# Kernel tuning notes

Measured on AMD Instinct MI355X. Metric: run time of the kernel, lower is better.

The kernel has to match this reference:

```python
import jax, jax.numpy as jnp
import numpy as np

COMMITMENT_COST = 0.25
DIST_SCALE = 400.0


def setup_inputs() -> dict:
    key = jax.random.key(0)
    ks = jax.random.split(key, 6)
    B, T, D, K = 64, 1024, 512, 512
    s = 1.0 / np.sqrt(D)
    return {
        "inputs": jax.random.normal(ks[0], (B, T, D), dtype=jnp.float32),
        "mean_W": jax.random.normal(ks[1], (D, D), dtype=jnp.float32) * s,
        "mean_b": jax.random.normal(ks[2], (D,), dtype=jnp.float32) * s,
        "logvar_W": jax.random.normal(ks[3], (D, K), dtype=jnp.float32) * s,
        "logvar_b": jax.random.normal(ks[4], (K,), dtype=jnp.float32) * s,
        "embedding": jax.random.normal(ks[5], (K, D), dtype=jnp.float32),
    }


def reference(inputs, mean_W, mean_b, logvar_W, logvar_b, embedding):
    sg = jax.lax.stop_gradient
    D = embedding.shape[1]
    flat = inputs.reshape(-1, D)                      # [N, D]
    x = flat @ mean_W + mean_b                        # mean_layer, [N, D]
    z_logvar = x @ logvar_W + logvar_b                # logvar_layer, [N, K]
    # squared euclidean distances to codebook, [N, K]
    distances = (
        jnp.sum(x * x, axis=1, keepdims=True)
        + jnp.sum(embedding * embedding, axis=1)
        - 2.0 * (x @ embedding.T)
    )
    smooth = jnp.exp(-2.0 * z_logvar)                 # 1/exp(logvar)^2
    d = distances / DIST_SCALE
    prob = jnp.exp(-d * (0.5 * smooth)) / jnp.sqrt(smooth)
    probs = prob / jnp.sum(prob, axis=1, keepdims=True)  # per-row normalize, [N, K]
    quantized = (probs @ embedding).reshape(inputs.shape)
    e_latent_loss = jnp.mean((sg(quantized) - inputs) ** 2)
    q_latent_loss = jnp.mean((quantized - sg(inputs)) ** 2)
    loss = q_latent_loss + COMMITMENT_COST * e_latent_loss
    quantized_st = inputs + sg(quantized - inputs)    # straight-through
    avg_probs = jnp.mean(probs, axis=0)
    perplexity = jnp.exp(-jnp.sum(avg_probs * jnp.log(avg_probs + 1e-10)))
    return loss, quantized_st, perplexity, probs
```

## Files before the change

### kernel.cpp

```cpp
#include <hip/hip_runtime.h>
#include <stdint.h>

#define BM 128
#define BN 128
#define BK 32
#define DIMD 512
#define NROWS 65536
#define QOFF 1
#define PERPOFF 33554433
#define PROBSOFF 33554434
#define NELEM 33554432

typedef __attribute__((ext_vector_type(8))) short bf16x8;
typedef __attribute__((ext_vector_type(4))) short s16x4;
typedef __attribute__((ext_vector_type(4))) float f32x4;

typedef const __attribute__((address_space(1))) void* gas_ptr;
typedef __attribute__((address_space(3))) void* las_ptr;

__device__ __forceinline__ short f2bf(float x){
  uint32_t u = __builtin_bit_cast(uint32_t, x);
  uint32_t r = (u + 0x7fffu + ((u >> 16) & 1u)) >> 16;
  return (short)(uint16_t)r;
}
__device__ __forceinline__ float bf2f(short h){
  return __builtin_bit_cast(float, ((uint32_t)(uint16_t)h) << 16);
}

__device__ __forceinline__ void stage_bf16(const short* __restrict__ g, int row0, int ld, int k0,
                                           short* lds){
  int tid = threadIdx.x;
#pragma unroll
  for (int i = 0; i < 2; ++i){
    int t = tid + i * 256;
    int row = t >> 2, c = t & 3;
    const short* src = g + (long)(row0 + row) * ld + k0 + c * 8;
    __builtin_amdgcn_global_load_lds((gas_ptr)src, (las_ptr)(lds + t * 8), 16, 0, 0);
  }
}

__device__ __forceinline__ void stage_f32_split(const float* __restrict__ g, int row0, int ld, int k0,
                                                short* hi, short* lo){
  int tid = threadIdx.x;
#pragma unroll
  for (int i = 0; i < 4; ++i){
    int t = tid + i * 256;
    int row = t >> 3, c = t & 7;
    const float4 v = *(const float4*)(g + (long)(row0 + row) * ld + k0 + c * 4);
    short h0 = f2bf(v.x), h1 = f2bf(v.y), h2 = f2bf(v.z), h3 = f2bf(v.w);
    s16x4 hv; hv[0] = h0; hv[1] = h1; hv[2] = h2; hv[3] = h3;
    s16x4 lv;
    lv[0] = f2bf(v.x - bf2f(h0)); lv[1] = f2bf(v.y - bf2f(h1));
    lv[2] = f2bf(v.z - bf2f(h2)); lv[3] = f2bf(v.w - bf2f(h3));
    *(s16x4*)(hi + row * BK + c * 4) = hv;
    *(s16x4*)(lo + row * BK + c * 4) = lv;
  }
}

__device__ __forceinline__ bf16x8 frag(const short* lds, int r, int q){
  return *(const bf16x8*)(lds + r * BK + q * 8);
}

__global__ __launch_bounds__(256) void k_convert_w(
    const float* __restrict__ meanW, const float* __restrict__ lvW, const float* __restrict__ emb,
    short* __restrict__ MWThi, short* __restrict__ MWTlo,
    short* __restrict__ VWThi, short* __restrict__ VWTlo,
    short* __restrict__ E, short* __restrict__ ET, float* __restrict__ enorm)
{
  int b = blockIdx.x;
  int tid = threadIdx.x;
  float esum = 0.f;
  for (int j = tid; j < 512; j += 256){
    float w = meanW[b * 512 + j];
    short h = f2bf(w); short l = f2bf(w - bf2f(h));
    MWThi[j * 512 + b] = h; MWTlo[j * 512 + b] = l;
    float v = lvW[b * 512 + j];
    h = f2bf(v); l = f2bf(v - bf2f(h));
    VWThi[j * 512 + b] = h; VWTlo[j * 512 + b] = l;
    float e = emb[b * 512 + j];
    short eh = f2bf(e);
    E[b * 512 + j] = eh;
    ET[j * 512 + b] = eh;
    esum += e * e;
  }
  for (int o = 32; o >= 1; o >>= 1) esum += __shfl_xor(esum, o);
  __shared__ float red[4];
  if ((tid & 63) == 0) red[tid >> 6] = esum;
  __syncthreads();
  if (tid == 0) enorm[b] = red[0] + red[1] + red[2] + red[3];
}

__global__ __launch_bounds__(256, 2) void k_gemm_mean(
    const float* __restrict__ inp, const short* __restrict__ Bhi, const short* __restrict__ Blo,
    const float* __restrict__ bias, short* __restrict__ Xhi, short* __restrict__ Xlo,
    float* __restrict__ xnorm)
{
  __shared__ short Ah[BM * BK], Al[BM * BK], Bh[BN * BK], Bl[BN * BK];
  int tid = threadIdx.x;
  int n0 = blockIdx.x * BM, c0 = blockIdx.y * BN;
  int lane = tid & 63, wid = tid >> 6;
  int wm = wid >> 1, wn = wid & 1;
  int q = lane >> 4, m = lane & 15;
  f32x4 acc[4][4];
#pragma unroll
  for (int i = 0; i < 4; i++)
#pragma unroll
    for (int j = 0; j < 4; j++)
#pragma unroll
      for (int r = 0; r < 4; r++) acc[i][j][r] = 0.f;

  for (int k0 = 0; k0 < DIMD; k0 += BK){
    __syncthreads();
    stage_f32_split(inp, n0, DIMD, k0, Ah, Al);
    stage_bf16(Bhi, c0, DIMD, k0, Bh);
    stage_bf16(Blo, c0, DIMD, k0, Bl);
    __syncthreads();
    bf16x8 ah[4], al[4], bh[4], bl[4];
#pragma unroll
    for (int i = 0; i < 4; i++){
      ah[i] = frag(Ah, wm * 64 + i * 16 + m, q);
      al[i] = frag(Al, wm * 64 + i * 16 + m, q);
      bh[i] = frag(Bh, wn * 64 + i * 16 + m, q);
      bl[i] = frag(Bl, wn * 64 + i * 16 + m, q);
    }
#pragma unroll
    for (int i = 0; i < 4; i++)
#pragma unroll
      for (int j = 0; j < 4; j++){
        acc[i][j] = __builtin_amdgcn_mfma_f32_16x16x32_bf16(ah[i], bh[j], acc[i][j], 0, 0, 0);
        acc[i][j] = __builtin_amdgcn_mfma_f32_16x16x32_bf16(ah[i], bl[j], acc[i][j], 0, 0, 0);
        acc[i][j] = __builtin_amdgcn_mfma_f32_16x16x32_bf16(al[i], bh[j], acc[i][j], 0, 0, 0);
      }
  }
#pragma unroll
  for (int i = 0; i < 4; i++){
#pragma unroll
    for (int r = 0; r < 4; r++){
      int row = n0 + wm * 64 + i * 16 + q * 4 + r;
      float xn = 0.f;
#pragma unroll
      for (int j = 0; j < 4; j++){
        int col = c0 + wn * 64 + j * 16 + m;
        float x = acc[i][j][r] + bias[col];
        short h = f2bf(x);
        short l = f2bf(x - bf2f(h));
        Xhi[(long)row * DIMD + col] = h;
        Xlo[(long)row * DIMD + col] = l;
        xn += x * x;
      }
      xn += __shfl_xor(xn, 1); xn += __shfl_xor(xn, 2);
      xn += __shfl_xor(xn, 4); xn += __shfl_xor(xn, 8);
      if (m == 0) atomicAdd(&xnorm[row], xn);
    }
  }
}

__global__ __launch_bounds__(256, 2) void k_gemm_logvar(
    const short* __restrict__ Xh, const short* __restrict__ Xl,
    const short* __restrict__ Bhi, const short* __restrict__ Blo,
    const float* __restrict__ bias, float* __restrict__ zlv)
{
  __shared__ short Ah[BM * BK], Al[BM * BK], Bh[BN * BK], Bl[BN * BK];
  int tid = threadIdx.x;
  int n0 = blockIdx.x * BM, c0 = blockIdx.y * BN;
  int lane = tid & 63, wid = tid >> 6;
  int wm = wid >> 1, wn = wid & 1;
  int q = lane >> 4, m = lane & 15;
  f32x4 acc[4][4];
#pragma unroll
  for (int i = 0; i < 4; i++)
#pragma unroll
    for (int j = 0; j < 4; j++)
#pragma unroll
      for (int r = 0; r < 4; r++) acc[i][j][r] = 0.f;

  for (int k0 = 0; k0 < DIMD; k0 += BK){
    __syncthreads();
    stage_bf16(Xh, n0, DIMD, k0, Ah);
    stage_bf16(Xl, n0, DIMD, k0, Al);
    stage_bf16(Bhi, c0, DIMD, k0, Bh);
    stage_bf16(Blo, c0, DIMD, k0, Bl);
    __syncthreads();
    bf16x8 ah[4], al[4], bh[4], bl[4];
#pragma unroll
    for (int i = 0; i < 4; i++){
      ah[i] = frag(Ah, wm * 64 + i * 16 + m, q);
      al[i] = frag(Al, wm * 64 + i * 16 + m, q);
      bh[i] = frag(Bh, wn * 64 + i * 16 + m, q);
      bl[i] = frag(Bl, wn * 64 + i * 16 + m, q);
    }
#pragma unroll
    for (int i = 0; i < 4; i++)
#pragma unroll
      for (int j = 0; j < 4; j++){
        acc[i][j] = __builtin_amdgcn_mfma_f32_16x16x32_bf16(ah[i], bh[j], acc[i][j], 0, 0, 0);
        acc[i][j] = __builtin_amdgcn_mfma_f32_16x16x32_bf16(ah[i], bl[j], acc[i][j], 0, 0, 0);
        acc[i][j] = __builtin_amdgcn_mfma_f32_16x16x32_bf16(al[i], bh[j], acc[i][j], 0, 0, 0);
      }
  }
#pragma unroll
  for (int i = 0; i < 4; i++)
#pragma unroll
    for (int r = 0; r < 4; r++){
      int row = n0 + wm * 64 + i * 16 + q * 4 + r;
#pragma unroll
      for (int j = 0; j < 4; j++){
        int col = c0 + wn * 64 + j * 16 + m;
        zlv[(long)row * DIMD + col] = acc[i][j][r] + bias[col];
      }
    }
}

__global__ __launch_bounds__(256, 2) void k_gemm_dist(
    const short* __restrict__ Xh, const short* __restrict__ E, float* __restrict__ S)
{
  __shared__ short Ah[BM * BK], Bh[BN * BK];
  int tid = threadIdx.x;
  int n0 = blockIdx.x * BM, c0 = blockIdx.y * BN;
  int lane = tid & 63, wid = tid >> 6;
  int wm = wid >> 1, wn = wid & 1;
  int q = lane >> 4, m = lane & 15;
  f32x4 acc[4][4];
#pragma unroll
  for (int i = 0; i < 4; i++)
#pragma unroll
    for (int j = 0; j < 4; j++)
#pragma unroll
      for (int r = 0; r < 4; r++) acc[i][j][r] = 0.f;

  for (int k0 = 0; k0 < DIMD; k0 += BK){
    __syncthreads();
    stage_bf16(Xh, n0, DIMD, k0, Ah);
    stage_bf16(E, c0, DIMD, k0, Bh);
    __syncthreads();
    bf16x8 a[4], b[4];
#pragma unroll
    for (int i = 0; i < 4; i++){
      a[i] = frag(Ah, wm * 64 + i * 16 + m, q);
      b[i] = frag(Bh, wn * 64 + i * 16 + m, q);
    }
#pragma unroll
    for (int i = 0; i < 4; i++)
#pragma unroll
      for (int j = 0; j < 4; j++)
        acc[i][j] = __builtin_amdgcn_mfma_f32_16x16x32_bf16(a[i], b[j], acc[i][j], 0, 0, 0);
  }
#pragma unroll
  for (int i = 0; i < 4; i++)
#pragma unroll
    for (int r = 0; r < 4; r++){
      int row = n0 + wm * 64 + i * 16 + q * 4 + r;
#pragma unroll
      for (int j = 0; j < 4; j++){
        int col = c0 + wn * 64 + j * 16 + m;
        S[(long)row * DIMD + col] = acc[i][j][r];
      }
    }
}

__global__ __launch_bounds__(256) void k_softmax(
    const float* __restrict__ zlv, const float* Sm, const float* __restrict__ xnorm,
    const float* __restrict__ enorm, float* probs_out, short* __restrict__ probs_bf,
    float* __restrict__ Pacc)
{
  __shared__ float red[4];
  int tid = threadIdx.x;
  int n0 = blockIdx.x * 32;
  int k1 = tid, k2 = tid + 256;
  float en1 = enorm[k1], en2 = enorm[k2];
  float pa1 = 0.f, pa2 = 0.f;
  const float inv400 = 1.0f / 400.0f;
  for (int r = 0; r < 32; ++r){
    long n = n0 + r;
    float xn = xnorm[n];
    float z1 = zlv[n * 512 + k1], z2 = zlv[n * 512 + k2];
    float s1 = Sm[n * 512 + k1],  s2 = Sm[n * 512 + k2];
    float sm1 = __expf(-2.f * z1), sm2 = __expf(-2.f * z2);
    float L1 = z1 - 0.5f * inv400 * (xn + en1 - 2.f * s1) * sm1;
    float L2 = z2 - 0.5f * inv400 * (xn + en2 - 2.f * s2) * sm2;
    float mx = fmaxf(L1, L2);
    for (int o = 32; o >= 1; o >>= 1) mx = fmaxf(mx, __shfl_xor(mx, o));
    if ((tid & 63) == 0) red[tid >> 6] = mx;
    __syncthreads();
    mx = fmaxf(fmaxf(red[0], red[1]), fmaxf(red[2], red[3]));
    __syncthreads();
    float p1 = __expf(L1 - mx), p2 = __expf(L2 - mx);
    float sm = p1 + p2;
    for (int o = 32; o >= 1; o >>= 1) sm += __shfl_xor(sm, o);
    if ((tid & 63) == 0) red[tid >> 6] = sm;
    __syncthreads();
    sm = red[0] + red[1] + red[2] + red[3];
    __syncthreads();
    float inv = 1.0f / sm;
    float q1 = p1 * inv, q2 = p2 * inv;
    probs_out[n * 512 + k1] = q1;
    probs_out[n * 512 + k2] = q2;
    probs_bf[n * 512 + k1] = f2bf(q1);
    probs_bf[n * 512 + k2] = f2bf(q2);
    pa1 += q1; pa2 += q2;
  }
  atomicAdd(&Pacc[k1], pa1);
  atomicAdd(&Pacc[k2], pa2);
}

__global__ __launch_bounds__(256, 2) void k_gemm_quant(
    const short* __restrict__ P, const short* __restrict__ ET,
    const float* __restrict__ inp, float* __restrict__ qout, float* __restrict__ lossacc)
{
  __shared__ short Ah[BM * BK], Bh[BN * BK];
  __shared__ float red[4];
  int tid = threadIdx.x;
  int n0 = blockIdx.x * BM, c0 = blockIdx.y * BN;
  int lane = tid & 63, wid = tid >> 6;
  int wm = wid >> 1, wn = wid & 1;
  int q = lane >> 4, m = lane & 15;
  f32x4 acc[4][4];
#pragma unroll
  for (int i = 0; i < 4; i++)
#pragma unroll
    for (int j = 0; j < 4; j++)
#pragma unroll
      for (int r = 0; r < 4; r++) acc[i][j][r] = 0.f;

  for (int k0 = 0; k0 < DIMD; k0 += BK){
    __syncthreads();
    stage_bf16(P, n0, DIMD, k0, Ah);
    stage_bf16(ET, c0, DIMD, k0, Bh);
    __syncthreads();
    bf16x8 a[4], b[4];
#pragma unroll
    for (int i = 0; i < 4; i++){
      a[i] = frag(Ah, wm * 64 + i * 16 + m, q);
      b[i] = frag(Bh, wn * 64 + i * 16 + m, q);
    }
#pragma unroll
    for (int i = 0; i < 4; i++)
#pragma unroll
      for (int j = 0; j < 4; j++)
        acc[i][j] = __builtin_amdgcn_mfma_f32_16x16x32_bf16(a[i], b[j], acc[i][j], 0, 0, 0);
  }
  float lsum = 0.f;
#pragma unroll
  for (int i = 0; i < 4; i++)
#pragma unroll
    for (int r = 0; r < 4; r++){
      int row = n0 + wm * 64 + i * 16 + q * 4 + r;
#pragma unroll
      for (int j = 0; j < 4; j++){
        int col = c0 + wn * 64 + j * 16 + m;
        float qv = acc[i][j][r];
        qout[(long)row * DIMD + col] = qv;
        float d = qv - inp[(long)row * DIMD + col];
        lsum += d * d;
      }
    }
  for (int o = 32; o >= 1; o >>= 1) lsum += __shfl_xor(lsum, o);
  if (lane == 0) red[wid] = lsum;
  __syncthreads();
  if (tid == 0) atomicAdd(lossacc, red[0] + red[1] + red[2] + red[3]);
}

__global__ __launch_bounds__(256) void k_final(
    const float* __restrict__ Pacc, const float* __restrict__ lossacc, float* __restrict__ out)
{
  int tid = threadIdx.x;
  float h = 0.f;
  for (int k = tid; k < 512; k += 256){
    float a = Pacc[k] * (1.0f / 65536.0f);
    h += a * __logf(a + 1e-10f);
  }
  for (int o = 32; o >= 1; o >>= 1) h += __shfl_xor(h, o);
  __shared__ float red[4];
  if ((tid & 63) == 0) red[tid >> 6] = h;
  __syncthreads();
  if (tid == 0){
    float H = red[0] + red[1] + red[2] + red[3];
    out[0] = 1.25f * lossacc[0] * (1.0f / (float)NELEM);
    out[PERPOFF] = __expf(-H);
  }
}

extern "C" void kernel_launch(void* const* d_in, const int* in_sizes, int n_in,
                              void* d_out, int out_size, void* d_ws, size_t ws_size,
                              hipStream_t stream)
{
  const float* inp   = (const float*)d_in[0];
  const float* meanW = (const float*)d_in[1];
  const float* meanb = (const float*)d_in[2];
  const float* lvW   = (const float*)d_in[3];
  const float* lvb   = (const float*)d_in[4];
  const float* emb   = (const float*)d_in[5];
  float* out = (float*)d_out;

  char* w = (char*)d_ws;
  short* Xhi = (short*)w;   w += (size_t)NROWS * DIMD * 2;
  short* Xlo = (short*)w;   w += (size_t)NROWS * DIMD * 2;
  short* MWThi = (short*)w; w += 512 * 512 * 2;
  short* MWTlo = (short*)w; w += 512 * 512 * 2;
  short* VWThi = (short*)w; w += 512 * 512 * 2;
  short* VWTlo = (short*)w; w += 512 * 512 * 2;
  short* E     = (short*)w; w += 512 * 512 * 2;
  short* ET    = (short*)w; w += 512 * 512 * 2;
  float* enorm = (float*)w; w += 512 * 4;
  float* stats = (float*)w;
  float* xnorm   = stats;
  float* Pacc    = stats + NROWS;
  float* lossacc = stats + NROWS + 512;

  float* zlv = out + QOFF;
  float* S   = out + PROBSOFF;

  hipMemsetAsync(stats, 0, (size_t)(NROWS + 512 + 16) * 4, stream);

  k_convert_w<<<512, 256, 0, stream>>>(meanW, lvW, emb, MWThi, MWTlo, VWThi, VWTlo, E, ET, enorm);
  k_gemm_mean<<<dim3(512, 4), 256, 0, stream>>>(inp, MWThi, MWTlo, meanb, Xhi, Xlo, xnorm);
  k_gemm_logvar<<<dim3(512, 4), 256, 0, stream>>>(Xhi, Xlo, VWThi, VWTlo, lvb, zlv);
  k_gemm_dist<<<dim3(512, 4), 256, 0, stream>>>(Xhi, E, S);
  k_softmax<<<2048, 256, 0, stream>>>(zlv, S, xnorm, enorm, out + PROBSOFF, Xlo, Pacc);
  k_gemm_quant<<<dim3(512, 4), 256, 0, stream>>>(Xlo, ET, inp, out + QOFF, lossacc);
  k_final<<<1, 256, 0, stream>>>(Pacc, lossacc, out);
}
```

Measured before the change: 865.8 us.

## Fuse logvar, distance, softmax and quantize GEMMs into one row-block kernel

Replaces four kernels (logvar GEMM, distance GEMM, softmax, quantize GEMM) with one kernel. Each 512-thread block owns 64 rows and all 512 columns, so z_logvar and the distance scores stay in registers, the softmax is reduced through LDS, and the bf16 probabilities are kept in swizzled LDS for the final GEMM. This removes the global round trips of z_logvar, S and the bf16 probs. It also adds async global_load_lds staging with XOR-swizzled LDS and loads issued one step ahead. The cost is about 108KB of LDS per block and two large accumulator sets per thread, which limits occupancy.

After: 784.4 us. -9.4%, faster.

```diff
diff --git a/kernel.cpp b/kernel.cpp
--- a/kernel.cpp
+++ b/kernel.cpp
@@ -59,6 +59,46 @@
 
 __device__ __forceinline__ bf16x8 frag(const short* lds, int r, int q){
   return *(const bf16x8*)(lds + r * BK + q * 8);
+}
+
+__device__ __forceinline__ int swz4(int row, int c){ return c ^ ((row >> 1) & 3); }
+
+__device__ __forceinline__ bf16x8 frag_s(const short* lds, int r, int q){
+  return *(const bf16x8*)(lds + r * BK + swz4(r, q) * 8);
+}
+
+__device__ __forceinline__ void stage_B512(const short* __restrict__ g, int k0, short* lds){
+  int tid = threadIdx.x;
+#pragma unroll
+  for (int i = 0; i < 4; ++i){
+    int t = tid + i * 512;
+    int row = t >> 2, c = t & 3;
+    int cs = swz4(row, c);
+    __builtin_amdgcn_global_load_lds((gas_ptr)(g + (long)row * DIMD + k0 + cs * 8),
+                                     (las_ptr)(lds + t * 8), 16, 0, 0);
+  }
+}
+
+__device__ __forceinline__ void stage_A64(const short* __restrict__ gh, const short* __restrict__ gl,
+                                          int n0, int k0, short* Ah, short* Al){
+  int tid = threadIdx.x;
+  int t = tid & 255;
+  int row = t >> 2, c = t & 3;
+  int cs = swz4(row, c);
+  const short* g = (tid < 256) ? gh : gl;
+  short* lds = (tid < 256) ? Ah : Al;
+  __builtin_amdgcn_global_load_lds((gas_ptr)(g + (long)(n0 + row) * DIMD + k0 + cs * 8),
+                                   (las_ptr)(lds + t * 8), 16, 0, 0);
+}
+
+__device__ __forceinline__ void stage_A64h(const short* __restrict__ g, int n0, int k0, short* Ah){
+  int tid = threadIdx.x;
+  if (tid < 256){
+    int row = tid >> 2, c = tid & 3;
+    int cs = swz4(row, c);
+    __builtin_amdgcn_global_load_lds((gas_ptr)(g + (long)(n0 + row) * DIMD + k0 + cs * 8),
+                                     (las_ptr)(Ah + tid * 8), 16, 0, 0);
+  }
 }
 
 __global__ __launch_bounds__(256) void k_convert_w(
@@ -155,209 +195,283 @@
   }
 }
 
-__global__ __launch_bounds__(256, 2) void k_gemm_logvar(
+__global__ __launch_bounds__(512, 2) void k_fused(
     const short* __restrict__ Xh, const short* __restrict__ Xl,
-    const short* __restrict__ Bhi, const short* __restrict__ Blo,
-    const float* __restrict__ bias, float* __restrict__ zlv)
+    const short* __restrict__ Vh, const short* __restrict__ Vl,
+    const short* __restrict__ Eb, const short* __restrict__ Et,
+    const float* __restrict__ lvb, const float* __restrict__ xnorm,
+    const float* __restrict__ enorm, const float* __restrict__ inp,
+    float* __restrict__ probs, float* __restrict__ qout,
+    float* __restrict__ Pacc, float* __restrict__ lossacc)
 {
-  __shared__ short Ah[BM * BK], Al[BM * BK], Bh[BN * BK], Bl[BN * BK];
-  int tid = threadIdx.x;
-  int n0 = blockIdx.x * BM, c0 = blockIdx.y * BN;
-  int lane = tid & 63, wid = tid >> 6;
-  int wm = wid >> 1, wn = wid & 1;
-  int q = lane >> 4, m = lane & 15;
-  f32x4 acc[4][4];
-#pragma unroll
-  for (int i = 0; i < 4; i++)
-#pragma unroll
-    for (int j = 0; j < 4; j++)
-#pragma unroll
-      for (int r = 0; r < 4; r++) acc[i][j][r] = 0.f;
-
-  for (int k0 = 0; k0 < DIMD; k0 += BK){
-    __syncthreads();
-    stage_bf16(Xh, n0, DIMD, k0, Ah);
-    stage_bf16(Xl, n0, DIMD, k0, Al);
-    stage_bf16(Bhi, c0, DIMD, k0, Bh);
-    stage_bf16(Blo, c0, DIMD, k0, Bl);
+  __shared__ __align__(128) char pool[110592];
+  short* Ah  = (short*)pool;
+  short* Al  = (short*)(pool + 4096);
+  short* Bv0 = (short*)(pool + 8192);
+  short* Bv1 = (short*)(pool + 40960);
+  short* Be  = (short*)(pool + 73728);
+  float* rrA = (float*)(pool + 106496);
+  float* rrB = (float*)(pool + 108544);
+  short* P   = (short*)(pool + 8192);
+
+  const int tid = threadIdx.x;
+  const int n0 = blockIdx.x * 64;
+  const int lane = tid & 63, wid = tid >> 6;
+  const int q = lane >> 4, m = lane & 15;
+  const int c0 = wid * 64;
+
+  f32x4 accZ[4][4];
+  f32x4 accS[4][4];
+#pragma unroll
+  for (int i = 0; i < 4; i++)
+#pragma unroll
+    for (int j = 0; j < 4; j++)
+#pragma unroll
+      for (int r = 0; r < 4; r++) accZ[i][j][r] = 0.f;
+
+  stage_A64(Xh, Xl, n0, 0, Ah, Al);
+  stage_B512(Vh, 0, Bv0);
+  stage_B512(Vl, 0, Bv1);
+  for (int k0 = 0; k0 < 512; k0 += 32){
     __syncthreads();
     bf16x8 ah[4], al[4], bh[4], bl[4];
 #pragma unroll
     for (int i = 0; i < 4; i++){
-      ah[i] = frag(Ah, wm * 64 + i * 16 + m, q);
-      al[i] = frag(Al, wm * 64 + i * 16 + m, q);
-      bh[i] = frag(Bh, wn * 64 + i * 16 + m, q);
-      bl[i] = frag(Bl, wn * 64 + i * 16 + m, q);
-    }
+      ah[i] = frag_s(Ah, i * 16 + m, q);
+      al[i] = frag_s(Al, i * 16 + m, q);
+    }
+#pragma unroll
+    for (int j = 0; j < 4; j++){
+      bh[j] = frag_s(Bv0, c0 + j * 16 + m, q);
+      bl[j] = frag_s(Bv1, c0 + j * 16 + m, q);
+    }
+    __syncthreads();
+    if (k0 < 480){
+      stage_A64(Xh, Xl, n0, k0 + 32, Ah, Al);
+      stage_B512(Vh, k0 + 32, Bv0);
+      stage_B512(Vl, k0 + 32, Bv1);
+    }
+#pragma unroll
+    for (int j = 0; j < 4; j++)
+#pragma unroll
+      for (int i = 0; i < 4; i++){
+        accZ[i][j] = __builtin_amdgcn_mfma_f32_16x16x32_bf16(ah[i], bh[j], accZ[i][j], 0, 0, 0);
+        accZ[i][j] = __builtin_amdgcn_mfma_f32_16x16x32_bf16(ah[i], bl[j], accZ[i][j], 0, 0, 0);
+        accZ[i][j] = __builtin_amdgcn_mfma_f32_16x16x32_bf16(al[i], bh[j], accZ[i][j], 0, 0, 0);
+      }
+  }
+
+#pragma unroll
+  for (int i = 0; i < 4; i++)
+#pragma unroll
+    for (int j = 0; j < 4; j++)
+#pragma unroll
+      for (int r = 0; r < 4; r++) accS[i][j][r] = 0.f;
+  stage_A64h(Xh, n0, 0, Ah);
+  stage_B512(Eb, 0, Be);
+  for (int k0 = 0; k0 < 512; k0 += 32){
+    __syncthreads();
+    bf16x8 ah[4], be[4];
+#pragma unroll
+    for (int i = 0; i < 4; i++) ah[i] = frag_s(Ah, i * 16 + m, q);
+#pragma unroll
+    for (int j = 0; j < 4; j++) be[j] = frag_s(Be, c0 + j * 16 + m, q);
+    __syncthreads();
+    if (k0 < 480){
+      stage_A64h(Xh, n0, k0 + 32, Ah);
+      stage_B512(Eb, k0 + 32, Be);
+    }
+#pragma unroll
+    for (int j = 0; j < 4; j++)
+#pragma unroll
+      for (int i = 0; i < 4; i++)
+        accS[i][j] = __builtin_amdgcn_mfma_f32_16x16x32_bf16(ah[i], be[j], accS[i][j], 0, 0, 0);
+  }
+
+  float lvbv[4], env[4];
+#pragma unroll
+  for (int j = 0; j < 4; j++){
+    int col = c0 + j * 16 + m;
+    lvbv[j] = lvb[col];
+    env[j] = enorm[col];
+  }
+  float xnv[4][4];
+#pragma unroll
+  for (int i = 0; i < 4; i++)
+#pragma unroll
+    for (int r = 0; r < 4; r++) xnv[i][r] = xnorm[n0 + i * 16 + q * 4 + r];
+
+  const float inv800 = 0.5f / 400.0f;
+#pragma unroll
+  for (int i = 0; i < 4; i++)
+#pragma unroll
+    for (int j = 0; j < 4; j++)
+#pragma unroll
+      for (int r = 0; r < 4; r++){
+        float z = accZ[i][j][r] + lvbv[j];
+        float s = accS[i][j][r];
+        float sm = __expf(-2.f * z);
+        accS[i][j][r] = z - inv800 * (xnv[i][r] + env[j] - 2.f * s) * sm;
+      }
+
+  float mxp[4][4];
+#pragma unroll
+  for (int i = 0; i < 4; i++)
+#pragma unroll
+    for (int r = 0; r < 4; r++){
+      float v = accS[i][0][r];
+#pragma unroll
+      for (int j = 1; j < 4; j++) v = fmaxf(v, accS[i][j][r]);
+      v = fmaxf(v, __shfl_xor(v, 1));
+      v = fmaxf(v, __shfl_xor(v, 2));
+      v = fmaxf(v, __shfl_xor(v, 4));
+      v = fmaxf(v, __shfl_xor(v, 8));
+      mxp[i][r] = v;
+    }
+  if (m == 0){
 #pragma unroll
     for (int i = 0; i < 4; i++)
 #pragma unroll
+      for (int r = 0; r < 4; r++)
+        rrA[(i * 16 + q * 4 + r) * 8 + wid] = mxp[i][r];
+  }
+  __syncthreads();
+  float mxf[4][4];
+#pragma unroll
+  for (int i = 0; i < 4; i++)
+#pragma unroll
+    for (int r = 0; r < 4; r++){
+      int row = i * 16 + q * 4 + r;
+      float v = rrA[row * 8 + 0];
+#pragma unroll
+      for (int w = 1; w < 8; w++) v = fmaxf(v, rrA[row * 8 + w]);
+      mxf[i][r] = v;
+    }
+
+  float smr[4][4];
+#pragma unroll
+  for (int i = 0; i < 4; i++)
+#pragma unroll
+    for (int r = 0; r < 4; r++){
+      float sacc = 0.f;
+#pragma unroll
       for (int j = 0; j < 4; j++){
-        acc[i][j] = __builtin_amdgcn_mfma_f32_16x16x32_bf16(ah[i], bh[j], acc[i][j], 0, 0, 0);
-        acc[i][j] = __builtin_amdgcn_mfma_f32_16x16x32_bf16(ah[i], bl[j], acc[i][j], 0, 0, 0);
-        acc[i][j] = __builtin_amdgcn_mfma_f32_16x16x32_bf16(al[i], bh[j], acc[i][j], 0, 0, 0);
-      }
-  }
-#pragma unroll
-  for (int i = 0; i < 4; i++)
-#pragma unroll
-    for (int r = 0; r < 4; r++){
-      int row = n0 + wm * 64 + i * 16 + q * 4 + r;
+        float p = __expf(accS[i][j][r] - mxf[i][r]);
+        accS[i][j][r] = p;
+        sacc += p;
+      }
+      sacc += __shfl_xor(sacc, 1);
+      sacc += __shfl_xor(sacc, 2);
+      sacc += __shfl_xor(sacc, 4);
+      sacc += __shfl_xor(sacc, 8);
+      smr[i][r] = sacc;
+    }
+  if (m == 0){
+#pragma unroll
+    for (int i = 0; i < 4; i++)
+#pragma unroll
+      for (int r = 0; r < 4; r++)
+        rrB[(i * 16 + q * 4 + r) * 8 + wid] = smr[i][r];
+  }
+  __syncthreads();
+#pragma unroll
+  for (int i = 0; i < 4; i++)
+#pragma unroll
+    for (int r = 0; r < 4; r++){
+      int row = i * 16 + q * 4 + r;
+      float v = 0.f;
+#pragma unroll
+      for (int w = 0; w < 8; w++) v += rrB[row * 8 + w];
+      smr[i][r] = v;
+    }
+
+  float pj[4];
+#pragma unroll
+  for (int j = 0; j < 4; j++) pj[j] = 0.f;
+#pragma unroll
+  for (int i = 0; i < 4; i++)
+#pragma unroll
+    for (int r = 0; r < 4; r++){
+      int rowl = i * 16 + q * 4 + r;
+      long rowg = n0 + rowl;
+      float inv = 1.0f / smr[i][r];
 #pragma unroll
       for (int j = 0; j < 4; j++){
-        int col = c0 + wn * 64 + j * 16 + m;
-        zlv[(long)row * DIMD + col] = acc[i][j][r] + bias[col];
-      }
-    }
-}
-
-__global__ __launch_bounds__(256, 2) void k_gemm_dist(
-    const short* __restrict__ Xh, const short* __restrict__ E, float* __restrict__ S)
-{
-  __shared__ short Ah[BM * BK], Bh[BN * BK];
-  int tid = threadIdx.x;
-  int n0 = blockIdx.x * BM, c0 = blockIdx.y * BN;
-  int lane = tid & 63, wid = tid >> 6;
-  int wm = wid >> 1, wn = wid & 1;
-  int q = lane >> 4, m = lane & 15;
-  f32x4 acc[4][4];
-#pragma unroll
-  for (int i = 0; i < 4; i++)
-#pragma unroll
-    for (int j = 0; j < 4; j++)
-#pragma unroll
-      for (int r = 0; r < 4; r++) acc[i][j][r] = 0.f;
-
-  for (int k0 = 0; k0 < DIMD; k0 += BK){
-    __syncthreads();
-    stage_bf16(Xh, n0, DIMD, k0, Ah);
-    stage_bf16(E, c0, DIMD, k0, Bh);
-    __syncthreads();
-    bf16x8 a[4], b[4];
+        int col = c0 + j * 16 + m;
+        float qv = accS[i][j][r] * inv;
+        probs[rowg * 512 + col] = qv;
+        pj[j] += qv;
+        int cg = col >> 3;
+        P[rowl * 512 + ((((cg ^ (rowl & 7)) << 3)) | (col & 7))] = f2bf(qv);
+      }
+    }
+#pragma unroll
+  for (int j = 0; j < 4; j++){
+    pj[j] += __shfl_xor(pj[j], 16);
+    pj[j] += __shfl_xor(pj[j], 32);
+  }
+  if (lane < 16){
+#pragma unroll
+    for (int j = 0; j < 4; j++) atomicAdd(&Pacc[c0 + j * 16 + m], pj[j]);
+  }
+
+#pragma unroll
+  for (int i = 0; i < 4; i++)
+#pragma unroll
+    for (int j = 0; j < 4; j++)
+#pragma unroll
+      for (int r = 0; r < 4; r++) accZ[i][j][r] = 0.f;
+  stage_B512(Et, 0, Be);
+  for (int k0 = 0; k0 < 512; k0 += 32){
+    __syncthreads();
+    bf16x8 pa[4], bq[4];
 #pragma unroll
     for (int i = 0; i < 4; i++){
-      a[i] = frag(Ah, wm * 64 + i * 16 + m, q);
-      b[i] = frag(Bh, wn * 64 + i * 16 + m, q);
-    }
-#pragma unroll
-    for (int i = 0; i < 4; i++)
-#pragma unroll
-      for (int j = 0; j < 4; j++)
-        acc[i][j] = __builtin_amdgcn_mfma_f32_16x16x32_bf16(a[i], b[j], acc[i][j], 0, 0, 0);
-  }
-#pragma unroll
-  for (int i = 0; i < 4; i++)
-#pragma unroll
-    for (int r = 0; r < 4; r++){
-      int row = n0 + wm * 64 + i * 16 + q * 4 + r;
+      int rowl = i * 16 + m;
+      int cg = (k0 >> 3) + q;
+      pa[i] = *(const bf16x8*)(P + rowl * 512 + ((cg ^ (rowl & 7)) << 3));
+    }
+#pragma unroll
+    for (int j = 0; j < 4; j++) bq[j] = frag_s(Be, c0 + j * 16 + m, q);
+    __syncthreads();
+    if (k0 < 480) stage_B512(Et, k0 + 32, Be);
+#pragma unroll
+    for (int j = 0; j < 4; j++)
+#pragma unroll
+      for (int i = 0; i < 4; i++)
+        accZ[i][j] = __builtin_amdgcn_mfma_f32_16x16x32_bf16(pa[i], bq[j], accZ[i][j], 0, 0, 0);
+  }
+
+  float lsum = 0.f;
+#pragma unroll
+  for (int i = 0; i < 4; i++)
+#pragma unroll
+    for (int r = 0; r < 4; r++){
+      long rowg = n0 + i * 16 + q * 4 + r;
 #pragma unroll
       for (int j = 0; j < 4; j++){
-        int col = c0 + wn * 64 + j * 16 + m;
-        S[(long)row * DIMD + col] = acc[i][j][r];
-      }
-    }
-}
-
-__global__ __launch_bounds__(256) void k_softmax(
-    const float* __restrict__ zlv, const float* Sm, const float* __restrict__ xnorm,
-    const float* __restrict__ enorm, float* probs_out, short* __restrict__ probs_bf,
-    float* __restrict__ Pacc)
-{
-  __shared__ float red[4];
-  int tid = threadIdx.x;
-  int n0 = blockIdx.x * 32;
-  int k1 = tid, k2 = tid + 256;
-  float en1 = enorm[k1], en2 = enorm[k2];
-  float pa1 = 0.f, pa2 = 0.f;
-  const float inv400 = 1.0f / 400.0f;
-  for (int r = 0; r < 32; ++r){
-    long n = n0 + r;
-    float xn = xnorm[n];
-    float z1 = zlv[n * 512 + k1], z2 = zlv[n * 512 + k2];
-    float s1 = Sm[n * 512 + k1],  s2 = Sm[n * 512 + k2];
-    float sm1 = __expf(-2.f * z1), sm2 = __expf(-2.f * z2);
-    float L1 = z1 - 0.5f * inv400 * (xn + en1 - 2.f * s1) * sm1;
-    float L2 = z2 - 0.5f * inv400 * (xn + en2 - 2.f * s2) * sm2;
-    float mx = fmaxf(L1, L2);
-    for (int o = 32; o >= 1; o >>= 1) mx = fmaxf(mx, __shfl_xor(mx, o));
-    if ((tid & 63) == 0) red[tid >> 6] = mx;
-    __syncthreads();
-    mx = fmaxf(fmaxf(red[0], red[1]), fmaxf(red[2], red[3]));
-    __syncthreads();
-    float p1 = __expf(L1 - mx), p2 = __expf(L2 - mx);
-    float sm = p1 + p2;
-    for (int o = 32; o >= 1; o >>= 1) sm += __shfl_xor(sm, o);
-    if ((tid & 63) == 0) red[tid >> 6] = sm;
-    __syncthreads();
-    sm = red[0] + red[1] + red[2] + red[3];
-    __syncthreads();
-    float inv = 1.0f / sm;
-    float q1 = p1 * inv, q2 = p2 * inv;
-    probs_out[n * 512 + k1] = q1;
-    probs_out[n * 512 + k2] = q2;
-    probs_bf[n * 512 + k1] = f2bf(q1);
-    probs_bf[n * 512 + k2] = f2bf(q2);
-    pa1 += q1; pa2 += q2;
-  }
-  atomicAdd(&Pacc[k1], pa1);
-  atomicAdd(&Pacc[k2], pa2);
-}
-
-__global__ __launch_bounds__(256, 2) void k_gemm_quant(
-    const short* __restrict__ P, const short* __restrict__ ET,
-    const float* __restrict__ inp, float* __restrict__ qout, float* __restrict__ lossacc)
-{
-  __shared__ short Ah[BM * BK], Bh[BN * BK];
-  __shared__ float red[4];
-  int tid = threadIdx.x;
-  int n0 = blockIdx.x * BM, c0 = blockIdx.y * BN;
-  int lane = tid & 63, wid = tid >> 6;
-  int wm = wid >> 1, wn = wid & 1;
-  int q = lane >> 4, m = lane & 15;
-  f32x4 acc[4][4];
-#pragma unroll
-  for (int i = 0; i < 4; i++)
-#pragma unroll
-    for (int j = 0; j < 4; j++)
-#pragma unroll
-      for (int r = 0; r < 4; r++) acc[i][j][r] = 0.f;
-
-  for (int k0 = 0; k0 < DIMD; k0 += BK){
-    __syncthreads();
-    stage_bf16(P, n0, DIMD, k0, Ah);
-    stage_bf16(ET, c0, DIMD, k0, Bh);
-    __syncthreads();
-    bf16x8 a[4], b[4];
-#pragma unroll
-    for (int i = 0; i < 4; i++){
-      a[i] = frag(Ah, wm * 64 + i * 16 + m, q);
-      b[i] = frag(Bh, wn * 64 + i * 16 + m, q);
-    }
-#pragma unroll
-    for (int i = 0; i < 4; i++)
-#pragma unroll
-      for (int j = 0; j < 4; j++)
-        acc[i][j] = __builtin_amdgcn_mfma_f32_16x16x32_bf16(a[i], b[j], acc[i][j], 0, 0, 0);
-  }
-  float lsum = 0.f;
-#pragma unroll
-  for (int i = 0; i < 4; i++)
-#pragma unroll
-    for (int r = 0; r < 4; r++){
-      int row = n0 + wm * 64 + i * 16 + q * 4 + r;
-#pragma unroll
-      for (int j = 0; j < 4; j++){
-        int col = c0 + wn * 64 + j * 16 + m;
-        float qv = acc[i][j][r];
-        qout[(long)row * DIMD + col] = qv;
-        float d = qv - inp[(long)row * DIMD + col];
+        int col = c0 + j * 16 + m;
+        float qv = accZ[i][j][r];
+        long idx = rowg * 512 + col;
+        qout[idx] = qv;
+        float d = qv - inp[idx];
         lsum += d * d;
       }
     }
-  for (int o = 32; o >= 1; o >>= 1) lsum += __shfl_xor(lsum, o);
-  if (lane == 0) red[wid] = lsum;
+  lsum += __shfl_xor(lsum, 32);
+  lsum += __shfl_xor(lsum, 16);
+  lsum += __shfl_xor(lsum, 8);
+  lsum += __shfl_xor(lsum, 4);
+  lsum += __shfl_xor(lsum, 2);
+  lsum += __shfl_xor(lsum, 1);
+  if (lane == 0) rrA[wid] = lsum;
   __syncthreads();
-  if (tid == 0) atomicAdd(lossacc, red[0] + red[1] + red[2] + red[3]);
+  if (tid == 0){
+    float t = 0.f;
+#pragma unroll
+    for (int w = 0; w < 8; w++) t += rrA[w];
+    atomicAdd(lossacc, t);
+  }
 }
 
 __global__ __launch_bounds__(256) void k_final(
@@ -407,16 +521,11 @@
   float* Pacc    = stats + NROWS;
   float* lossacc = stats + NROWS + 512;
 
-  float* zlv = out + QOFF;
-  float* S   = out + PROBSOFF;
-
   hipMemsetAsync(stats, 0, (size_t)(NROWS + 512 + 16) * 4, stream);
 
   k_convert_w<<<512, 256, 0, stream>>>(meanW, lvW, emb, MWThi, MWTlo, VWThi, VWTlo, E, ET, enorm);
   k_gemm_mean<<<dim3(512, 4), 256, 0, stream>>>(inp, MWThi, MWTlo, meanb, Xhi, Xlo, xnorm);
-  k_gemm_logvar<<<dim3(512, 4), 256, 0, stream>>>(Xhi, Xlo, VWThi, VWTlo, lvb, zlv);
-  k_gemm_dist<<<dim3(512, 4), 256, 0, stream>>>(Xhi, E, S);
-  k_softmax<<<2048, 256, 0, stream>>>(zlv, S, xnorm, enorm, out + PROBSOFF, Xlo, Pacc);
-  k_gemm_quant<<<dim3(512, 4), 256, 0, stream>>>(Xlo, ET, inp, out + QOFF, lossacc);
+  k_fused<<<1024, 512, 0, stream>>>(Xhi, Xlo, VWThi, VWTlo, E, ET, lvb, xnorm, enorm, inp,
+                                    out + PROBSOFF, out + QOFF, Pacc, lossacc);
   k_final<<<1, 256, 0, stream>>>(Pacc, lossacc, out);
 }
```
